# Optimization experiments

Hardware: AMD Instinct MI355X
Metric: run time of the kernel (lower is better)

## Reference

```python
import jax, jax.numpy as jnp
import numpy as np

B, T, H, OUT_STEPS, D = 131072, 51, 64, 20, 4


def setup_inputs() -> dict:
    key = jax.random.key(0)
    ks = jax.random.split(key, 11)
    s = 1.0 / np.sqrt(H)  # torch nn.GRU / nn.Linear uniform init bound
    u = lambda k, shape: jax.random.uniform(k, shape, jnp.float32, -s, s)
    return {
        "input_seq": jax.random.normal(ks[0], (B, T, D), jnp.float32),
        "enc_Wih": u(ks[1], (3 * H, D)),
        "enc_Whh": u(ks[2], (3 * H, H)),
        "enc_bih": u(ks[3], (3 * H,)),
        "enc_bhh": u(ks[4], (3 * H,)),
        "dec_Wih": u(ks[5], (3 * H, D)),
        "dec_Whh": u(ks[6], (3 * H, H)),
        "dec_bih": u(ks[7], (3 * H,)),
        "dec_bhh": u(ks[8], (3 * H,)),
        "lin_W": u(ks[9], (D, H)),
        "lin_b": u(ks[10], (D,)),
    }


def _gru_cell(x, h, Wih, Whh, bih, bhh):
    """PyTorch GRU cell semantics. x: [B,D_in], h: [B,H]."""
    gi = x @ Wih.T + bih  # [B,3H]
    gh = h @ Whh.T + bhh  # [B,3H]
    ir, iz, inn = jnp.split(gi, 3, axis=-1)
    hr, hz, hn = jnp.split(gh, 3, axis=-1)
    r = jax.nn.sigmoid(ir + hr)
    z = jax.nn.sigmoid(iz + hz)
    n = jnp.tanh(inn + r * hn)
    return (1.0 - z) * n + z * h


def reference(input_seq, enc_Wih, enc_Whh, enc_bih, enc_bhh,
              dec_Wih, dec_Whh, dec_bih, dec_bhh, lin_W, lin_b):
    # offset: last observed point, broadcast over the 20 output steps
    offset = input_seq[:, -1:, :]  # [B,1,D]
    diffs = input_seq[:, 1:] - input_seq[:, :-1]  # [B,T-1,D]; dropout p=0 -> identity
    h0 = jnp.zeros((input_seq.shape[0], H), input_seq.dtype)

    def enc_step(h, x_t):
        return _gru_cell(x_t, h, enc_Wih, enc_Whh, enc_bih, enc_bhh), None

    hn, _ = jax.lax.scan(enc_step, h0, jnp.swapaxes(diffs, 0, 1))  # final hidden [B,H]

    def dec_step(carry, _):
        h, px = carry
        h = _gru_cell(px, h, dec_Wih, dec_Whh, dec_bih, dec_bhh)
        x = h @ lin_W.T + lin_b + px  # linear + residual
        return (h, x), x

    _, xs = jax.lax.scan(dec_step, (hn, diffs[:, -1]), None, length=OUT_STEPS)
    out = jnp.swapaxes(xs, 0, 1)  # [B,OUT_STEPS,D]
    return out + offset
```

## Files before the change

### kernel.cpp

```cpp
#include <hip/hip_runtime.h>
#include <hip/hip_bf16.h>

namespace {

constexpr int kT = 51;
constexpr int kOut = 20;
constexpr float kL2E  = 1.4426950408889634f;
constexpr float kL2E2 = 2.8853900817779268f;

typedef __attribute__((ext_vector_type(8))) short bf16x8;
typedef __attribute__((ext_vector_type(4))) float f32x4;

union FragU {
    bf16x8 v;
    unsigned long long u64[2];
    unsigned int u32[4];
    unsigned short s[8];
};

__device__ __forceinline__ unsigned short f2bf(float x) {
    union { float f; unsigned int u; } v;
    v.f = x;
    unsigned int r = (v.u + 0x7fffu + ((v.u >> 16) & 1u)) >> 16;
    return (unsigned short)r;
}

__device__ __forceinline__ unsigned int packbf(float a, float b) {
    union { float f; unsigned int u; } ua, ub;
    ua.f = a; ub.f = b;
    return __builtin_amdgcn_perm(ub.u + 0x8000u, ua.u + 0x8000u, 0x07060302u);
}

__global__ __launch_bounds__(256, 3) void gru_encdec(
    const float* __restrict__ input,
    const float* __restrict__ eWih, const float* __restrict__ eWhh,
    const float* __restrict__ ebih, const float* __restrict__ ebhh,
    const float* __restrict__ dWih, const float* __restrict__ dWhh,
    const float* __restrict__ dbih, const float* __restrict__ dbhh,
    const float* __restrict__ linW, const float* __restrict__ linb,
    float* __restrict__ out)
{
    __shared__ __align__(16) unsigned short hbuf[2][2][16 * 68];
    __shared__ __align__(16) float sout[2][16 * 84];

    const int lane = (int)(threadIdx.x & 63u);
    const int wid = (int)(threadIdx.x >> 6u);
    const int p = wid >> 1;
    const int w = wid & 1;
    const int q = lane >> 4;
    const int i = lane & 15;
    const long b = (long)blockIdx.x * 32 + p * 16 + i;
    const float* __restrict__ xrow = input + b * (kT * 4);
    const bool q0 = (q == 0);

    bf16x8 WA[6][2];
    bf16x8 WAUG[6];
    f32x4 bhhn4[2];
    float hprev[8];
    bf16x8 bh0 = {0, 0, 0, 0, 0, 0, 0, 0};
    bf16x8 bh1 = {0, 0, 0, 0, 0, 0, 0, 0};
    float px[4];
    const f32x4 z4 = {0.f, 0.f, 0.f, 0.f};
    int sel = 0;

    auto gtile = [&](int l) -> int {
        return (l < 2) ? (2 * w + l) : (l < 4) ? (4 + 2 * w + l - 2)
                                               : (8 + 2 * w + l - 4);
    };

    auto load_whh = [&](const float* __restrict__ Whh) {
#pragma unroll
        for (int l = 0; l < 6; ++l) {
            const int tau = gtile(l);
            const float sc = (l < 4) ? kL2E : kL2E2;
#pragma unroll
            for (int f = 0; f < 2; ++f) {
                const float* ptr = Whh + (tau * 16 + i) * 64 + f * 32 + q * 8;
                FragU fu;
#pragma unroll
                for (int j = 0; j < 8; ++j) fu.s[j] = f2bf(ptr[j] * sc);
                WA[l][f] = fu.v;
            }
        }
    };

    auto load_aug = [&](const float* __restrict__ Wih,
                        const float* __restrict__ bih,
                        const float* __restrict__ bhh) {
#pragma unroll
        for (int l = 0; l < 6; ++l) {
            const int tau = gtile(l);
            const float sc = (l < 4) ? kL2E : kL2E2;
            FragU fu;
            fu.u64[0] = 0; fu.u64[1] = 0;
            if (q0) {
                int j = tau * 16 + i;
#pragma unroll
                for (int d = 0; d < 4; ++d) fu.s[d] = f2bf(Wih[j * 4 + d] * sc);
                float bias = (l < 4) ? (bih[j] + bhh[j]) : bih[j];
                fu.s[4] = f2bf(bias * sc);
            }
            WAUG[l] = fu.v;
        }
#pragma unroll
        for (int t = 0; t < 2; ++t)
#pragma unroll
            for (int r = 0; r < 4; ++r)
                bhhn4[t][r] = bhh[128 + 32 * w + 16 * t + 4 * q + r] * kL2E2;
    };

    auto make_baug = [&]() -> bf16x8 {
        FragU fu;
        unsigned int p01 = packbf(px[0], px[1]);
        unsigned int p23 = packbf(px[2], px[3]);
        fu.u32[0] = q0 ? p01 : 0u;
        fu.u32[1] = q0 ? p23 : 0u;
        fu.u32[2] = q0 ? 0x3f80u : 0u;
        fu.u32[3] = 0u;
        return fu.v;
    };

    auto gru_step = [&](bf16x8 baug) {
        unsigned short* __restrict__ hw = hbuf[p][sel];
#pragma unroll
        for (int t = 0; t < 2; ++t) {
            f32x4 accR = __builtin_amdgcn_mfma_f32_16x16x32_bf16(WAUG[t], baug, z4, 0, 0, 0);
            accR = __builtin_amdgcn_mfma_f32_16x16x32_bf16(WA[t][0], bh0, accR, 0, 0, 0);
            accR = __builtin_amdgcn_mfma_f32_16x16x32_bf16(WA[t][1], bh1, accR, 0, 0, 0);
            f32x4 accZ = __builtin_amdgcn_mfma_f32_16x16x32_bf16(WAUG[2 + t], baug, z4, 0, 0, 0);
            accZ = __builtin_amdgcn_mfma_f32_16x16x32_bf16(WA[2 + t][0], bh0, accZ, 0, 0, 0);
            accZ = __builtin_amdgcn_mfma_f32_16x16x32_bf16(WA[2 + t][1], bh1, accZ, 0, 0, 0);
            f32x4 accNi = __builtin_amdgcn_mfma_f32_16x16x32_bf16(WAUG[4 + t], baug, z4, 0, 0, 0);
            f32x4 accNh = __builtin_amdgcn_mfma_f32_16x16x32_bf16(WA[4 + t][0], bh0, bhhn4[t], 0, 0, 0);
            accNh = __builtin_amdgcn_mfma_f32_16x16x32_bf16(WA[4 + t][1], bh1, accNh, 0, 0, 0);

            float hv[4];
#pragma unroll
            for (int r = 0; r < 4; ++r) {
                float rr = __builtin_amdgcn_rcpf(1.f + __builtin_amdgcn_exp2f(-accR[r]));
                float zz = __builtin_amdgcn_rcpf(1.f + __builtin_amdgcn_exp2f(-accZ[r]));
                float pre2 = __builtin_fmaf(rr, accNh[r], accNi[r]);
                float tt = __builtin_amdgcn_rcpf(__builtin_amdgcn_exp2f(pre2) + 1.f);
                float nn = __builtin_fmaf(-2.f, tt, 1.f);
                float hp = hprev[t * 4 + r];
                hv[r] = __builtin_fmaf(zz, hp - nn, nn);
                hprev[t * 4 + r] = hv[r];
            }
            uint2 wv;
            wv.x = packbf(hv[0], hv[1]);
            wv.y = packbf(hv[2], hv[3]);
            *(uint2*)&hw[i * 68 + 32 * w + 16 * t + 4 * q] = wv;
        }
        __syncthreads();
        FragU f0, f1;
        f0.u64[0] = *(const unsigned long long*)&hw[i * 68 + 8 * q];
        f0.u64[1] = *(const unsigned long long*)&hw[i * 68 + 8 * q + 4];
        f1.u64[0] = *(const unsigned long long*)&hw[i * 68 + 32 + 8 * q];
        f1.u64[1] = *(const unsigned long long*)&hw[i * 68 + 32 + 8 * q + 4];
        bh0 = f0.v;
        bh1 = f1.v;
        sel ^= 1;
    };

#pragma unroll
    for (int t = 0; t < 8; ++t) hprev[t] = 0.f;
    load_whh(eWhh);
    load_aug(eWih, ebih, ebhh);

    float4 xp = *(const float4*)(xrow);
    float4 xn = *(const float4*)(xrow + 4);
#pragma unroll 1
    for (int s = 0; s < kT - 1; ++s) {
        int idx = s + 2; if (idx > kT - 1) idx = kT - 1;
        float4 xf = *(const float4*)(xrow + idx * 4);
        px[0] = xn.x - xp.x;
        px[1] = xn.y - xp.y;
        px[2] = xn.z - xp.z;
        px[3] = xn.w - xp.w;
        gru_step(make_baug());
        xp = xn;
        xn = xf;
    }
    float4 offv = xp;

    load_whh(dWhh);
    load_aug(dWih, dbih, dbhh);

    bf16x8 AL0, AL1, AL2;
    {
        FragU a0, a1, a2;
        a0.u64[0] = a0.u64[1] = 0;
        a1.u64[0] = a1.u64[1] = 0;
        a2.u64[0] = a2.u64[1] = 0;
        if (i < 4) {
            const float* p0 = linW + i * 64 + q * 8;
            const float* p1 = linW + i * 64 + 32 + q * 8;
#pragma unroll
            for (int j = 0; j < 8; ++j) {
                a0.s[j] = f2bf(p0[j]);
                a1.s[j] = f2bf(p1[j]);
            }
            if (q0) a2.s[4] = f2bf(linb[i]);
        }
        AL0 = a0.v; AL1 = a1.v; AL2 = a2.v;
    }
    float* __restrict__ so = sout[p];

#pragma unroll 1
    for (int s = 0; s < kOut; ++s) {
        bf16x8 baug = make_baug();
        gru_step(baug);
        f32x4 accX = __builtin_amdgcn_mfma_f32_16x16x32_bf16(AL2, baug, z4, 0, 0, 0);
        accX = __builtin_amdgcn_mfma_f32_16x16x32_bf16(AL0, bh0, accX, 0, 0, 0);
        accX = __builtin_amdgcn_mfma_f32_16x16x32_bf16(AL1, bh1, accX, 0, 0, 0);
        float x0 = accX[0] + px[0];
        float x1 = accX[1] + px[1];
        float x2 = accX[2] + px[2];
        float x3 = accX[3] + px[3];
        if (w == 0 && q0) {
            float* sr = so + i * 84 + s * 4;
            sr[0] = x0 + offv.x;
            sr[1] = x1 + offv.y;
            sr[2] = x2 + offv.z;
            sr[3] = x3 + offv.w;
        }
        px[0] = x0; px[1] = x1; px[2] = x2; px[3] = x3;
    }

    if (w == 0) {
        float* __restrict__ go = out + ((long)blockIdx.x * 32 + p * 16) * (kOut * 4);
#pragma unroll
        for (int it = 0; it < 5; ++it) {
            int g = it * 256 + lane * 4;
            int row = g / 80;
            int e = g - row * 80;
            float4 v = *(const float4*)&so[row * 84 + e];
            *(float4*)&go[g] = v;
        }
    }
}

}

extern "C" void kernel_launch(void* const* d_in, const int* in_sizes, int n_in,
                              void* d_out, int out_size, void* d_ws, size_t ws_size,
                              hipStream_t stream) {
    const float* input = (const float*)d_in[0];
    const float* eWih = (const float*)d_in[1];
    const float* eWhh = (const float*)d_in[2];
    const float* ebih = (const float*)d_in[3];
    const float* ebhh = (const float*)d_in[4];
    const float* dWih = (const float*)d_in[5];
    const float* dWhh = (const float*)d_in[6];
    const float* dbih = (const float*)d_in[7];
    const float* dbhh = (const float*)d_in[8];
    const float* linW = (const float*)d_in[9];
    const float* linb = (const float*)d_in[10];
    float* out = (float*)d_out;

    const int B = in_sizes[0] / (kT * 4);
    const int nblocks = B / 32;
    gru_encdec<<<nblocks, 256, 0, stream>>>(input, eWih, eWhh, ebih, ebhh,
                                            dWih, dWhh, dbih, dbhh,
                                            linW, linb, out);
}
```

Baseline: 686.0 us.

## Split each 16-row batch tile across four waves and share one reciprocal for gates

Each block now handles 16 batch rows instead of 32. The four waves each own one 16-column slice of the r, z and n gates, where before two waves split each 16-row group. This halves the per-wave weight registers and MFMA chain per step, and the launch bound is raised to 4 blocks per SM for more occupancy. The r and z sigmoids now share a single reciprocal of the product of their denominators. In exchange there are twice as many blocks, each step's barrier waits on four waves with less work each, and the product trick adds a small risk of overflow for large gate preactivations.

Measured after the change: 691.8 us. No clear change (+0.8%).

```diff
diff --git a/kernel.cpp b/kernel.cpp
--- a/kernel.cpp
+++ b/kernel.cpp
@@ -31,7 +31,7 @@
     return __builtin_amdgcn_perm(ub.u + 0x8000u, ua.u + 0x8000u, 0x07060302u);
 }
 
-__global__ __launch_bounds__(256, 3) void gru_encdec(
+__global__ __launch_bounds__(256, 4) void gru_encdec(
     const float* __restrict__ input,
     const float* __restrict__ eWih, const float* __restrict__ eWhh,
     const float* __restrict__ ebih, const float* __restrict__ ebhh,
@@ -40,39 +40,32 @@
     const float* __restrict__ linW, const float* __restrict__ linb,
     float* __restrict__ out)
 {
-    __shared__ __align__(16) unsigned short hbuf[2][2][16 * 68];
-    __shared__ __align__(16) float sout[2][16 * 84];
+    __shared__ __align__(16) unsigned short hbuf[2][16 * 68];
+    __shared__ __align__(16) float sout[16 * 84];
 
     const int lane = (int)(threadIdx.x & 63u);
-    const int wid = (int)(threadIdx.x >> 6u);
-    const int p = wid >> 1;
-    const int w = wid & 1;
+    const int w = (int)(threadIdx.x >> 6u);
     const int q = lane >> 4;
     const int i = lane & 15;
-    const long b = (long)blockIdx.x * 32 + p * 16 + i;
+    const long b = (long)blockIdx.x * 16 + i;
     const float* __restrict__ xrow = input + b * (kT * 4);
     const bool q0 = (q == 0);
 
-    bf16x8 WA[6][2];
-    bf16x8 WAUG[6];
-    f32x4 bhhn4[2];
-    float hprev[8];
+    bf16x8 WA[3][2];
+    bf16x8 WAUG[3];
+    f32x4 bhhn4;
+    float hprev[4];
     bf16x8 bh0 = {0, 0, 0, 0, 0, 0, 0, 0};
     bf16x8 bh1 = {0, 0, 0, 0, 0, 0, 0, 0};
     float px[4];
     const f32x4 z4 = {0.f, 0.f, 0.f, 0.f};
     int sel = 0;
 
-    auto gtile = [&](int l) -> int {
-        return (l < 2) ? (2 * w + l) : (l < 4) ? (4 + 2 * w + l - 2)
-                                               : (8 + 2 * w + l - 4);
-    };
-
     auto load_whh = [&](const float* __restrict__ Whh) {
 #pragma unroll
-        for (int l = 0; l < 6; ++l) {
-            const int tau = gtile(l);
-            const float sc = (l < 4) ? kL2E : kL2E2;
+        for (int l = 0; l < 3; ++l) {
+            const int tau = 4 * l + w;
+            const float sc = (l < 2) ? kL2E : kL2E2;
 #pragma unroll
             for (int f = 0; f < 2; ++f) {
                 const float* ptr = Whh + (tau * 16 + i) * 64 + f * 32 + q * 8;
@@ -88,25 +81,23 @@
                         const float* __restrict__ bih,
                         const float* __restrict__ bhh) {
 #pragma unroll
-        for (int l = 0; l < 6; ++l) {
-            const int tau = gtile(l);
-            const float sc = (l < 4) ? kL2E : kL2E2;
+        for (int l = 0; l < 3; ++l) {
+            const int tau = 4 * l + w;
+            const float sc = (l < 2) ? kL2E : kL2E2;
             FragU fu;
             fu.u64[0] = 0; fu.u64[1] = 0;
             if (q0) {
                 int j = tau * 16 + i;
 #pragma unroll
                 for (int d = 0; d < 4; ++d) fu.s[d] = f2bf(Wih[j * 4 + d] * sc);
-                float bias = (l < 4) ? (bih[j] + bhh[j]) : bih[j];
+                float bias = (l < 2) ? (bih[j] + bhh[j]) : bih[j];
                 fu.s[4] = f2bf(bias * sc);
             }
             WAUG[l] = fu.v;
         }
 #pragma unroll
-        for (int t = 0; t < 2; ++t)
-#pragma unroll
-            for (int r = 0; r < 4; ++r)
-                bhhn4[t][r] = bhh[128 + 32 * w + 16 * t + 4 * q + r] * kL2E2;
+        for (int r = 0; r < 4; ++r)
+            bhhn4[r] = bhh[128 + 16 * w + 4 * q + r] * kL2E2;
     };
 
     auto make_baug = [&]() -> bf16x8 {
@@ -121,36 +112,39 @@
     };
 
     auto gru_step = [&](bf16x8 baug) {
-        unsigned short* __restrict__ hw = hbuf[p][sel];
-#pragma unroll
-        for (int t = 0; t < 2; ++t) {
-            f32x4 accR = __builtin_amdgcn_mfma_f32_16x16x32_bf16(WAUG[t], baug, z4, 0, 0, 0);
-            accR = __builtin_amdgcn_mfma_f32_16x16x32_bf16(WA[t][0], bh0, accR, 0, 0, 0);
-            accR = __builtin_amdgcn_mfma_f32_16x16x32_bf16(WA[t][1], bh1, accR, 0, 0, 0);
-            f32x4 accZ = __builtin_amdgcn_mfma_f32_16x16x32_bf16(WAUG[2 + t], baug, z4, 0, 0, 0);
-            accZ = __builtin_amdgcn_mfma_f32_16x16x32_bf16(WA[2 + t][0], bh0, accZ, 0, 0, 0);
-            accZ = __builtin_amdgcn_mfma_f32_16x16x32_bf16(WA[2 + t][1], bh1, accZ, 0, 0, 0);
-            f32x4 accNi = __builtin_amdgcn_mfma_f32_16x16x32_bf16(WAUG[4 + t], baug, z4, 0, 0, 0);
-            f32x4 accNh = __builtin_amdgcn_mfma_f32_16x16x32_bf16(WA[4 + t][0], bh0, bhhn4[t], 0, 0, 0);
-            accNh = __builtin_amdgcn_mfma_f32_16x16x32_bf16(WA[4 + t][1], bh1, accNh, 0, 0, 0);
-
-            float hv[4];
-#pragma unroll
-            for (int r = 0; r < 4; ++r) {
-                float rr = __builtin_amdgcn_rcpf(1.f + __builtin_amdgcn_exp2f(-accR[r]));
-                float zz = __builtin_amdgcn_rcpf(1.f + __builtin_amdgcn_exp2f(-accZ[r]));
-                float pre2 = __builtin_fmaf(rr, accNh[r], accNi[r]);
-                float tt = __builtin_amdgcn_rcpf(__builtin_amdgcn_exp2f(pre2) + 1.f);
-                float nn = __builtin_fmaf(-2.f, tt, 1.f);
-                float hp = hprev[t * 4 + r];
-                hv[r] = __builtin_fmaf(zz, hp - nn, nn);
-                hprev[t * 4 + r] = hv[r];
-            }
-            uint2 wv;
-            wv.x = packbf(hv[0], hv[1]);
-            wv.y = packbf(hv[2], hv[3]);
-            *(uint2*)&hw[i * 68 + 32 * w + 16 * t + 4 * q] = wv;
-        }
+        unsigned short* __restrict__ hw = hbuf[sel];
+        f32x4 accR = __builtin_amdgcn_mfma_f32_16x16x32_bf16(WAUG[0], baug, z4, 0, 0, 0);
+        accR = __builtin_amdgcn_mfma_f32_16x16x32_bf16(WA[0][0], bh0, accR, 0, 0, 0);
+        accR = __builtin_amdgcn_mfma_f32_16x16x32_bf16(WA[0][1], bh1, accR, 0, 0, 0);
+        f32x4 accZ = __builtin_amdgcn_mfma_f32_16x16x32_bf16(WAUG[1], baug, z4, 0, 0, 0);
+        accZ = __builtin_amdgcn_mfma_f32_16x16x32_bf16(WA[1][0], bh0, accZ, 0, 0, 0);
+        accZ = __builtin_amdgcn_mfma_f32_16x16x32_bf16(WA[1][1], bh1, accZ, 0, 0, 0);
+        f32x4 accNi = __builtin_amdgcn_mfma_f32_16x16x32_bf16(WAUG[2], baug, z4, 0, 0, 0);
+        f32x4 accNh = __builtin_amdgcn_mfma_f32_16x16x32_bf16(WA[2][0], bh0, bhhn4, 0, 0, 0);
+        accNh = __builtin_amdgcn_mfma_f32_16x16x32_bf16(WA[2][1], bh1, accNh, 0, 0, 0);
+
+        float hv[4];
+#pragma unroll
+        for (int r = 0; r < 4; ++r) {
+            float a = __builtin_amdgcn_exp2f(-accR[r]);
+            float bb = __builtin_amdgcn_exp2f(-accZ[r]);
+            float A = 1.f + a;
+            float Bv = 1.f + bb;
+            float rp = __builtin_amdgcn_rcpf(A * Bv);
+            float rr = rp * Bv;
+            float zz = rp * A;
+            float pre2 = __builtin_fmaf(rr, accNh[r], accNi[r]);
+            float tt = __builtin_amdgcn_rcpf(__builtin_amdgcn_exp2f(pre2) + 1.f);
+            float nn = __builtin_fmaf(-2.f, tt, 1.f);
+            float hp = hprev[r];
+            hv[r] = __builtin_fmaf(zz, hp - nn, nn);
+            hprev[r] = hv[r];
+        }
+        uint2 wv;
+        wv.x = packbf(hv[0], hv[1]);
+        wv.y = packbf(hv[2], hv[3]);
+        *(uint2*)&hw[i * 68 + 16 * w + 4 * q] = wv;
+
         __syncthreads();
         FragU f0, f1;
         f0.u64[0] = *(const unsigned long long*)&hw[i * 68 + 8 * q];
@@ -163,7 +157,7 @@
     };
 
 #pragma unroll
-    for (int t = 0; t < 8; ++t) hprev[t] = 0.f;
+    for (int r = 0; r < 4; ++r) hprev[r] = 0.f;
     load_whh(eWhh);
     load_aug(eWih, ebih, ebhh);
 
@@ -204,7 +198,6 @@
         }
         AL0 = a0.v; AL1 = a1.v; AL2 = a2.v;
     }
-    float* __restrict__ so = sout[p];
 
 #pragma unroll 1
     for (int s = 0; s < kOut; ++s) {
@@ -218,7 +211,7 @@
         float x2 = accX[2] + px[2];
         float x3 = accX[3] + px[3];
         if (w == 0 && q0) {
-            float* sr = so + i * 84 + s * 4;
+            float* sr = sout + i * 84 + s * 4;
             sr[0] = x0 + offv.x;
             sr[1] = x1 + offv.y;
             sr[2] = x2 + offv.z;
@@ -228,13 +221,13 @@
     }
 
     if (w == 0) {
-        float* __restrict__ go = out + ((long)blockIdx.x * 32 + p * 16) * (kOut * 4);
+        float* __restrict__ go = out + (long)blockIdx.x * 16 * (kOut * 4);
 #pragma unroll
         for (int it = 0; it < 5; ++it) {
             int g = it * 256 + lane * 4;
             int row = g / 80;
             int e = g - row * 80;
-            float4 v = *(const float4*)&so[row * 84 + e];
+            float4 v = *(const float4*)&sout[row * 84 + e];
             *(float4*)&go[g] = v;
         }
     }
@@ -259,7 +252,7 @@
     float* out = (float*)d_out;
 
     const int B = in_sizes[0] / (kT * 4);
-    const int nblocks = B / 32;
+    const int nblocks = B / 16;
     gru_encdec<<<nblocks, 256, 0, stream>>>(input, eWih, eWhh, ebih, ebhh,
                                             dWih, dWhh, dbih, dbhh,
                                             linW, linb, out);
```
